# Kernel tuning notes

Hardware: AMD Instinct MI355X
Metric: run time of the kernel (lower is better)

## Reference

```python
import jax, jax.numpy as jnp
import numpy as np

EMBED = 256
HEADS = 8
LEVELS = 3
POINTS = 4
MLP = 4
SS = np.array([[100, 100], [50, 50], [25, 25]], np.int32)  # (H, W) per level


def setup_inputs() -> dict:
    key = jax.random.key(0)
    ks = jax.random.split(key, 12)
    B, Q = 2, 128 * 128
    NV = int((SS[:, 0] * SS[:, 1]).sum())
    C = EMBED
    F = C * MLP
    s = 0.02

    def w(k, shape):
        return jax.random.normal(k, shape, jnp.float32) * s

    return dict(
        query=jax.random.normal(ks[0], (B, Q, C), jnp.float32),
        value=jax.random.normal(ks[1], (B, NV, C), jnp.float32),
        query_pos=jax.random.normal(ks[2], (B, Q, C), jnp.float32),
        ref_pts=jax.random.uniform(ks[3], (B, Q, 2), jnp.float32),
        spatial_shapes=SS,
        level_start_index=np.concatenate([[0], np.cumsum(SS[:, 0] * SS[:, 1])[:-1]]).astype(np.int32),
        ln1_g=jnp.ones(C), ln1_b=jnp.zeros(C),
        ln2_g=jnp.ones(C), ln2_b=jnp.zeros(C),
        W_value=w(ks[4], (C, C)), b_value=jnp.zeros(C),
        W_off=w(ks[5], (C, HEADS * LEVELS * POINTS * 2)), b_off=w(ks[6], (HEADS * LEVELS * POINTS * 2,)),
        W_attn=w(ks[7], (C, HEADS * LEVELS * POINTS)), b_attn=jnp.zeros(HEADS * LEVELS * POINTS),
        W_out=w(ks[8], (C, C)), b_out=jnp.zeros(C),
        W_ffn1=w(ks[9], (C, F)), b_ffn1=jnp.zeros(F),
        W_ffn2=w(ks[10], (F, C)), b_ffn2=jnp.zeros(C),
    )


def _layernorm(x, g, b, eps=1e-5):
    m = x.mean(-1, keepdims=True)
    v = ((x - m) ** 2).mean(-1, keepdims=True)
    return (x - m) * jax.lax.rsqrt(v + eps) * g + b


def _bilinear(v, loc, Hl, Wl):
    # v: [BH, Hl*Wl, d]; loc: [BH, Q, P, 2] normalized to [0,1].
    # grid_sample(align_corners=False, padding=zeros): pixel = loc*size - 0.5
    BH, Q, P, _ = loc.shape
    d = v.shape[-1]
    x = loc[..., 0] * Wl - 0.5
    y = loc[..., 1] * Hl - 0.5
    x0f = jnp.floor(x)
    y0f = jnp.floor(y)
    lx = x - x0f
    ly = y - y0f
    x0 = x0f.astype(jnp.int32)
    y0 = y0f.astype(jnp.int32)

    def gather(xi, yi):
        valid = ((xi >= 0) & (xi < Wl) & (yi >= 0) & (yi < Hl)).astype(v.dtype)
        idx = jnp.clip(yi, 0, Hl - 1) * Wl + jnp.clip(xi, 0, Wl - 1)
        g = jnp.take_along_axis(v, idx.reshape(BH, Q * P, 1), axis=1).reshape(BH, Q, P, d)
        return g * valid[..., None]

    w00 = (1 - lx) * (1 - ly)
    w01 = lx * (1 - ly)
    w10 = (1 - lx) * ly
    w11 = lx * ly
    return (gather(x0, y0) * w00[..., None] + gather(x0 + 1, y0) * w01[..., None]
            + gather(x0, y0 + 1) * w10[..., None] + gather(x0 + 1, y0 + 1) * w11[..., None])


def _forward(query, value, query_pos, ref_pts, spatial_shapes,
             ln1_g, ln1_b, ln2_g, ln2_b,
             W_value, b_value, W_off, b_off, W_attn, b_attn, W_out, b_out,
             W_ffn1, b_ffn1, W_ffn2, b_ffn2):
    B, Q, C = query.shape
    Hh, L, P = HEADS, LEVELS, POINTS
    d = C // Hh
    ss = np.asarray(spatial_shapes)
    starts = np.concatenate([[0], np.cumsum(ss[:, 0] * ss[:, 1])])

    # pre-norm + positional embedding (MSDeformAttn adds query_pos)
    qn = _layernorm(query, ln1_g, ln1_b)
    q = qn + query_pos

    # value projection, split heads
    v = (value @ W_value + b_value).reshape(B, -1, Hh, d)

    off = (q @ W_off + b_off).reshape(B, Q, Hh, L, P, 2)
    aw = jax.nn.softmax((q @ W_attn + b_attn).reshape(B, Q, Hh, L * P), axis=-1)
    aw = aw.reshape(B, Q, Hh, L, P)

    # offset normalizer is (W, H) per level
    normalizer = jnp.asarray(ss[:, ::-1].copy(), jnp.float32)
    # bev_value path: ref_pts broadcast over levels
    loc = ref_pts[:, :, None, None, None, :] + off / normalizer[None, None, None, :, None, :]

    out = jnp.zeros((B * Hh, Q, d), query.dtype)
    for l in range(L):
        Hl, Wl = int(ss[l, 0]), int(ss[l, 1])
        v_l = v[:, starts[l]:starts[l + 1]].transpose(0, 2, 1, 3).reshape(B * Hh, Hl * Wl, d)
        loc_l = loc[:, :, :, l].transpose(0, 2, 1, 3, 4).reshape(B * Hh, Q, P, 2)
        sampled = _bilinear(v_l, loc_l, Hl, Wl)  # [BH, Q, P, d]
        w_l = aw[:, :, :, l].transpose(0, 2, 1, 3).reshape(B * Hh, Q, P)
        out = out + (sampled * w_l[..., None]).sum(2)

    out = out.reshape(B, Hh, Q, d).transpose(0, 2, 1, 3).reshape(B, Q, C)
    x = query + (out @ W_out + b_out)

    h = _layernorm(x, ln2_g, ln2_b)
    x = x + (jax.nn.gelu(h @ W_ffn1 + b_ffn1, approximate=False) @ W_ffn2 + b_ffn2)
    return x


def reference(query, value, query_pos, ref_pts, spatial_shapes, level_start_index,
              ln1_g, ln1_b, ln2_g, ln2_b,
              W_value, b_value, W_off, b_off, W_attn, b_attn, W_out, b_out,
              W_ffn1, b_ffn1, W_ffn2, b_ffn2):
    return _forward(query, value, query_pos, ref_pts, spatial_shapes,
                    ln1_g, ln1_b, ln2_g, ln2_b,
                    W_value, b_value, W_off, b_off, W_attn, b_attn, W_out, b_out,
                    W_ffn1, b_ffn1, W_ffn2, b_ffn2)
```

## Files before the change

### kernel.cpp

```cpp
#include <hip/hip_runtime.h>
#include <hip/hip_bf16.h>

#define BQ      2
#define QLEN    16384
#define CDIM    256
#define HEADS   8
#define LEV     3
#define PTS     4
#define DHEAD   32
#define NVTOT   13125
#define FDIM    1024
#define NTOK    (BQ*QLEN)
#define MROWS_V (BQ*NVTOT)
#define NPROJ   288

typedef __attribute__((ext_vector_type(8))) short short8;
typedef __attribute__((ext_vector_type(4))) float floatx4;
typedef unsigned long long u64;

typedef const __attribute__((address_space(1))) unsigned int gu32;
typedef __attribute__((address_space(3))) unsigned int lu32;

__device__ __forceinline__ int imin(int a, int b){ return a<b?a:b; }
__device__ __forceinline__ int imax(int a, int b){ return a>b?a:b; }

__device__ __forceinline__ float bf2f(unsigned short u){ return __uint_as_float((unsigned)u << 16); }
__device__ __forceinline__ unsigned short f2bf(float f)
{
    __hip_bfloat16 h = __float2bfloat16(f);
    return *(unsigned short*)&h;
}
__device__ __forceinline__ u64 pack4(float4 v)
{
    return (u64)f2bf(v.x) | ((u64)f2bf(v.y) << 16)
         | ((u64)f2bf(v.z) << 32) | ((u64)f2bf(v.w) << 48);
}
__device__ __forceinline__ float4 unpack4(u64 c)
{
    float4 v;
    v.x = bf2f((unsigned short)(c));
    v.y = bf2f((unsigned short)(c >> 16));
    v.z = bf2f((unsigned short)(c >> 32));
    v.w = bf2f((unsigned short)(c >> 48));
    return v;
}

__device__ __forceinline__ float gelu_f(float x)
{
    float u2 = x * x;
    float a  = x * fmaf(0.0713548163f, u2, 1.5957691216f);
    float e  = __expf(a);
    float r  = __builtin_amdgcn_rcpf(e + 1.0f);
    return fmaf(-x, r, x);
}

__device__ __forceinline__ void ln_core(float4 v, const float* __restrict__ pos, int tok,
                                        const float* __restrict__ g, const float* __restrict__ b,
                                        int lane, __hip_bfloat16* __restrict__ out)
{
    float s = v.x + v.y + v.z + v.w;
    #pragma unroll
    for (int o = 32; o > 0; o >>= 1) s += __shfl_down(s, o);
    s = __shfl(s, 0);
    float mean = s * (1.0f / 256.0f);
    float4 c; c.x = v.x - mean; c.y = v.y - mean; c.z = v.z - mean; c.w = v.w - mean;
    float q2 = c.x*c.x + c.y*c.y + c.z*c.z + c.w*c.w;
    #pragma unroll
    for (int o = 32; o > 0; o >>= 1) q2 += __shfl_down(q2, o);
    q2 = __shfl(q2, 0);
    float rstd = rsqrtf(q2 * (1.0f / 256.0f) + 1e-5f);
    float4 gg = ((const float4*)g)[lane];
    float4 bb = ((const float4*)b)[lane];
    float4 o4;
    o4.x = c.x * rstd * gg.x + bb.x;
    o4.y = c.y * rstd * gg.y + bb.y;
    o4.z = c.z * rstd * gg.z + bb.z;
    o4.w = c.w * rstd * gg.w + bb.w;
    if (pos) {
        float4 p = ((const float4*)(pos + (size_t)tok * CDIM))[lane];
        o4.x += p.x; o4.y += p.y; o4.z += p.z; o4.w += p.w;
    }
    *(u64*)(out + (size_t)tok * CDIM + lane * 4) = pack4(o4);
}

#define WT_BLOCKS  2946
#define CVT_BLOCKS 6563
#define LN_BLOCKS  8192

__global__ __launch_bounds__(256)
void prep_k(const float* __restrict__ Wv,  const float* __restrict__ Woff,
            const float* __restrict__ Wat, const float* __restrict__ Wout,
            const float* __restrict__ W1,  const float* __restrict__ W2,
            const float* __restrict__ boff, const float* __restrict__ bat,
            const float* __restrict__ value, const float* __restrict__ query,
            const float* __restrict__ qpos,  const float* __restrict__ ln1g,
            const float* __restrict__ ln1b,
            __hip_bfloat16* __restrict__ o_v,  __hip_bfloat16* __restrict__ o_c,
            __hip_bfloat16* __restrict__ o_out,
            __hip_bfloat16* __restrict__ o_1,  __hip_bfloat16* __restrict__ o_2,
            float* __restrict__ o_bc,
            __hip_bfloat16* __restrict__ vbf,  __hip_bfloat16* __restrict__ qbf)
{
    int bx = blockIdx.x;
    if (bx < WT_BLOCKS) {
        int gid = bx * 256 + threadIdx.x;
        if (gid < 65536) {
            int idx = gid, n = idx >> 8, k = idx & 255;
            o_v[idx] = __float2bfloat16(Wv[(size_t)k * 256 + n]);
        } else if (gid < 163840) {
            int idx = gid - 65536, n = idx >> 8, k = idx & 255;
            float v = 0.0f;
            if (n < 192)       v = Woff[(size_t)k * 192 + n];
            else if (n < 288)  v = Wat[(size_t)k * 96 + (n - 192)];
            o_c[idx] = __float2bfloat16(v);
        } else if (gid < 229376) {
            int idx = gid - 163840, n = idx >> 8, k = idx & 255;
            o_out[idx] = __float2bfloat16(Wout[(size_t)k * 256 + n]);
        } else if (gid < 491520) {
            int idx = gid - 229376, n = idx >> 8, k = idx & 255;
            o_1[idx] = __float2bfloat16(W1[(size_t)k * 1024 + n]);
        } else if (gid < 753664) {
            int idx = gid - 491520, n = idx >> 10, k = idx & 1023;
            o_2[idx] = __float2bfloat16(W2[(size_t)k * 256 + n]);
        } else if (gid < 753952) {
            int idx = gid - 753664;
            o_bc[idx] = (idx < 192) ? boff[idx] : bat[idx - 192];
        }
    } else if (bx < WT_BLOCKS + CVT_BLOCKS) {
        int i = (bx - WT_BLOCKS) * 256 + threadIdx.x;
        if (i < MROWS_V * CDIM / 4) {
            float4 v = ((const float4*)value)[i];
            *(u64*)(vbf + (size_t)i * 4) = pack4(v);
        }
    } else {
        int tok  = (bx - WT_BLOCKS - CVT_BLOCKS) * 4 + (threadIdx.x >> 6);
        int lane = threadIdx.x & 63;
        float4 v = ((const float4*)(query + (size_t)tok * CDIM))[lane];
        ln_core(v, qpos, tok, ln1g, ln1b, lane, qbf);
    }
}

__global__ __launch_bounds__(256)
void ln2_k(const __hip_bfloat16* __restrict__ x, const float* __restrict__ g,
           const float* __restrict__ b, __hip_bfloat16* __restrict__ out)
{
    int tok  = blockIdx.x * 4 + (threadIdx.x >> 6);
    int lane = threadIdx.x & 63;
    float4 v = unpack4(((const u64*)(x + (size_t)tok * CDIM))[lane]);
    ln_core(v, nullptr, tok, g, b, lane, out);
}

enum { EP_PLAIN_BF16 = 0, EP_GELU_BF16 = 1, EP_RES_F2BF = 2, EP_RES_BF2F = 3 };

__global__ __launch_bounds__(256)
void mm_k(const __hip_bfloat16* __restrict__ A, const __hip_bfloat16* __restrict__ Bt,
          const float* __restrict__ bias, const void* __restrict__ res,
          void* __restrict__ Cout, int M, int N, int K, int mode)
{
    __shared__ float4 smem4[2048];
    __hip_bfloat16* Ws = (__hip_bfloat16*)smem4;
    __hip_bfloat16* Ts = (__hip_bfloat16*)smem4 + 128*64;
    u64* st = (u64*)smem4;
    int t = threadIdx.x;
    int lane = t & 63;
    int wave = t >> 6;
    int wm = wave >> 1, wn = wave & 1;
    int lm = lane & 15, lk = lane >> 4;
    int m0 = blockIdx.x * 128;
    int n0 = blockIdx.y * 128;

    floatx4 acc[4][4];
    #pragma unroll
    for (int i = 0; i < 4; i++)
        #pragma unroll
        for (int j = 0; j < 4; j++) acc[i][j] = (floatx4)0.0f;

    for (int kt = 0; kt < K; kt += 64) {
        #pragma unroll
        for (int i = 0; i < 4; i++) {
            int cc  = i * 256 + t;
            int row = cc >> 3;
            int c   = cc & 7;
            int kc  = c ^ (row & 7);
            int ra  = m0 + row; if (ra >= M) ra = M - 1;
            const __hip_bfloat16* gw = Bt + (size_t)(n0 + row) * K + kt + kc * 8;
            const __hip_bfloat16* gt = A  + (size_t)ra * K + kt + kc * 8;
            __builtin_amdgcn_global_load_lds((gu32*)gw, (lu32*)(Ws + cc * 8), 16, 0, 0);
            __builtin_amdgcn_global_load_lds((gu32*)gt, (lu32*)(Ts + cc * 8), 16, 0, 0);
        }
        __syncthreads();
        #pragma unroll
        for (int ks = 0; ks < 2; ks++) {
            short8 wf[4], tf[4];
            #pragma unroll
            for (int i = 0; i < 4; i++) {
                int rw = wn * 64 + i * 16 + lm;
                int cw = (ks * 4 + lk) ^ (rw & 7);
                wf[i] = *(const short8*)(Ws + (rw * 8 + cw) * 8);
                int rt = wm * 64 + i * 16 + lm;
                int ct = (ks * 4 + lk) ^ (rt & 7);
                tf[i] = *(const short8*)(Ts + (rt * 8 + ct) * 8);
            }
            #pragma unroll
            for (int i = 0; i < 4; i++)
                #pragma unroll
                for (int j = 0; j < 4; j++)
                    acc[i][j] = __builtin_amdgcn_mfma_f32_16x16x32_bf16(wf[i], tf[j], acc[i][j], 0, 0, 0);
        }
        __syncthreads();
    }

    #pragma unroll
    for (int i = 0; i < 4; i++) {
        int chan = n0 + wn * 64 + i * 16 + lk * 4;
        float4 b4 = make_float4(0.f, 0.f, 0.f, 0.f);
        if (chan < N) b4 = *(const float4*)(bias + chan);
        int c4 = wn * 16 + i * 4 + lk;
        #pragma unroll
        for (int j = 0; j < 4; j++) {
            int tl = wm * 64 + j * 16 + lm;
            float4 v;
            v.x = acc[i][j][0] + b4.x;
            v.y = acc[i][j][1] + b4.y;
            v.z = acc[i][j][2] + b4.z;
            v.w = acc[i][j][3] + b4.w;
            st[tl * 32 + (c4 ^ (tl & 31))] = pack4(v);
        }
    }
    __syncthreads();

    int rel = (t & 31) * 4;
    int c4r = t & 31;
    #pragma unroll
    for (int it = 0; it < 16; it++) {
        int tl   = it * 8 + (t >> 5);
        int tok  = m0 + tl;
        int chan = n0 + rel;
        if (tok >= M || chan >= N) continue;
        u64 chunk = st[tl * 32 + (c4r ^ (tl & 31))];
        if (mode == EP_PLAIN_BF16) {
            *(u64*)((__hip_bfloat16*)Cout + (size_t)tok * N + chan) = chunk;
        } else if (mode == EP_GELU_BF16) {
            float4 v = unpack4(chunk);
            v.x = gelu_f(v.x); v.y = gelu_f(v.y); v.z = gelu_f(v.z); v.w = gelu_f(v.w);
            *(u64*)((__hip_bfloat16*)Cout + (size_t)tok * N + chan) = pack4(v);
        } else if (mode == EP_RES_F2BF) {
            float4 v = unpack4(chunk);
            float4 rr = *(const float4*)((const float*)res + (size_t)tok * N + chan);
            v.x += rr.x; v.y += rr.y; v.z += rr.z; v.w += rr.w;
            *(u64*)((__hip_bfloat16*)Cout + (size_t)tok * N + chan) = pack4(v);
        } else {
            float4 v = unpack4(chunk);
            float4 rr = unpack4(*(const u64*)((const __hip_bfloat16*)res + (size_t)tok * N + chan));
            v.x += rr.x; v.y += rr.y; v.z += rr.z; v.w += rr.w;
            *(float4*)((float*)Cout + (size_t)tok * N + chan) = v;
        }
    }
}

__global__ __launch_bounds__(256)
void sample_k(const __hip_bfloat16* __restrict__ v, const __hip_bfloat16* __restrict__ cbuf,
              const float* __restrict__ ref, __hip_bfloat16* __restrict__ out)
{
    __shared__ int4   metaIdx[4 * 104];
    __shared__ float4 metaW[4 * 104];

    int wid  = threadIdx.x >> 6;
    int lane = threadIdx.x & 63;
    int t    = blockIdx.x * 4 + wid;
    int b    = t >> 14;
    float rx = ref[(size_t)t * 2 + 0];
    float ry = ref[(size_t)t * 2 + 1];
    const __hip_bfloat16* crow = cbuf + (size_t)t * NPROJ;

    #pragma unroll
    for (int rnd = 0; rnd < 2; rnd++) {
        int slot = rnd * 64 + lane;
        int h = slot >> 4, p = slot & 15;
        int pc = imin(p, 11);
        unsigned upk = *(const unsigned*)(crow + h * 24 + pc * 2);
        float ox = bf2f((unsigned short)upk);
        float oy = bf2f((unsigned short)(upk >> 16));
        float logit = bf2f(*(const unsigned short*)(crow + 192 + h * 12 + pc));
        float mx = logit;
        #pragma unroll
        for (int o = 8; o > 0; o >>= 1) mx = fmaxf(mx, __shfl_xor(mx, o, 16));
        float e = (p < 12) ? __expf(logit - mx) : 0.0f;
        float ssum = e;
        #pragma unroll
        for (int o = 8; o > 0; o >>= 1) ssum += __shfl_xor(ssum, o, 16);
        float aw = e * __builtin_amdgcn_rcpf(ssum);

        if (p < 12) {
            int l = p >> 2;
            float fS = (l == 0) ? 100.0f : ((l == 1) ? 50.0f : 25.0f);
            int   Wl = (l == 0) ? 100 : ((l == 1) ? 50 : 25);
            int   st = (l == 0) ? 0 : ((l == 1) ? 10000 : 12500);
            float x = fmaf(rx, fS, ox) - 0.5f;
            float y = fmaf(ry, fS, oy) - 0.5f;
            float x0f = floorf(x), y0f = floorf(y);
            float fx = x - x0f, fy = y - y0f;
            int x0 = (int)x0f, y0 = (int)y0f;
            int x1 = x0 + 1,  y1 = y0 + 1;
            int cx0 = imin(imax(x0, 0), Wl - 1), cx1 = imin(imax(x1, 0), Wl - 1);
            int cy0 = imin(imax(y0, 0), Wl - 1), cy1 = imin(imax(y1, 0), Wl - 1);
            float vx0 = (x0 >= 0 && x0 < Wl) ? 1.0f : 0.0f;
            float vx1 = (x1 >= 0 && x1 < Wl) ? 1.0f : 0.0f;
            float vy0 = (y0 >= 0 && y0 < Wl) ? 1.0f : 0.0f;
            float vy1 = (y1 >= 0 && y1 < Wl) ? 1.0f : 0.0f;
            int s = wid * 104 + h * 13 + p;
            metaIdx[s] = make_int4((st + cy0 * Wl + cx0) << 9, (st + cy0 * Wl + cx1) << 9,
                                   (st + cy1 * Wl + cx0) << 9, (st + cy1 * Wl + cx1) << 9);
            metaW[s] = make_float4((1.0f - fx) * (1.0f - fy) * aw * vx0 * vy0,
                                   fx * (1.0f - fy) * aw * vx1 * vy0,
                                   (1.0f - fx) * fy * aw * vx0 * vy1,
                                   fx * fy * aw * vx1 * vy1);
        }
    }
    __syncthreads();

    int h  = lane >> 3;
    int bs = __builtin_amdgcn_readfirstlane(b);
    const char* vb = (const char*)(v + (size_t)bs * NVTOT * CDIM);
    int hoff = lane * 8;
    float4 acc = {0.0f, 0.0f, 0.0f, 0.0f};
    #pragma unroll
    for (int p = 0; p < 12; p++) {
        int s = wid * 104 + h * 13 + p;
        int4   mi = metaIdx[s];
        float4 mw = metaW[s];
        u64 g0 = *(const u64*)(vb + (unsigned)(mi.x + hoff));
        u64 g1 = *(const u64*)(vb + (unsigned)(mi.y + hoff));
        u64 g2 = *(const u64*)(vb + (unsigned)(mi.z + hoff));
        u64 g3 = *(const u64*)(vb + (unsigned)(mi.w + hoff));
        {
            unsigned d0 = (unsigned)g0, d1 = (unsigned)(g0 >> 32);
            acc.x = fmaf(mw.x, __uint_as_float(d0 << 16), acc.x);
            acc.y = fmaf(mw.x, __uint_as_float(d0 & 0xffff0000u), acc.y);
            acc.z = fmaf(mw.x, __uint_as_float(d1 << 16), acc.z);
            acc.w = fmaf(mw.x, __uint_as_float(d1 & 0xffff0000u), acc.w);
        }
        {
            unsigned d0 = (unsigned)g1, d1 = (unsigned)(g1 >> 32);
            acc.x = fmaf(mw.y, __uint_as_float(d0 << 16), acc.x);
            acc.y = fmaf(mw.y, __uint_as_float(d0 & 0xffff0000u), acc.y);
            acc.z = fmaf(mw.y, __uint_as_float(d1 << 16), acc.z);
            acc.w = fmaf(mw.y, __uint_as_float(d1 & 0xffff0000u), acc.w);
        }
        {
            unsigned d0 = (unsigned)g2, d1 = (unsigned)(g2 >> 32);
            acc.x = fmaf(mw.z, __uint_as_float(d0 << 16), acc.x);
            acc.y = fmaf(mw.z, __uint_as_float(d0 & 0xffff0000u), acc.y);
            acc.z = fmaf(mw.z, __uint_as_float(d1 << 16), acc.z);
            acc.w = fmaf(mw.z, __uint_as_float(d1 & 0xffff0000u), acc.w);
        }
        {
            unsigned d0 = (unsigned)g3, d1 = (unsigned)(g3 >> 32);
            acc.x = fmaf(mw.w, __uint_as_float(d0 << 16), acc.x);
            acc.y = fmaf(mw.w, __uint_as_float(d0 & 0xffff0000u), acc.y);
            acc.z = fmaf(mw.w, __uint_as_float(d1 << 16), acc.z);
            acc.w = fmaf(mw.w, __uint_as_float(d1 & 0xffff0000u), acc.w);
        }
    }
    *(u64*)(out + (size_t)t * CDIM + lane * 4) = pack4(acc);
}

extern "C" void kernel_launch(void* const* d_in, const int* in_sizes, int n_in,
                              void* d_out, int out_size, void* d_ws, size_t ws_size,
                              hipStream_t stream)
{
    const float* query = (const float*)d_in[0];
    const float* value = (const float*)d_in[1];
    const float* qpos  = (const float*)d_in[2];
    const float* ref   = (const float*)d_in[3];
    const float* ln1g  = (const float*)d_in[6];
    const float* ln1b  = (const float*)d_in[7];
    const float* ln2g  = (const float*)d_in[8];
    const float* ln2b  = (const float*)d_in[9];
    const float* Wv    = (const float*)d_in[10];
    const float* bv    = (const float*)d_in[11];
    const float* Woff  = (const float*)d_in[12];
    const float* boff  = (const float*)d_in[13];
    const float* Wat   = (const float*)d_in[14];
    const float* bat   = (const float*)d_in[15];
    const float* Wout  = (const float*)d_in[16];
    const float* bout  = (const float*)d_in[17];
    const float* W1    = (const float*)d_in[18];
    const float* b1    = (const float*)d_in[19];
    const float* W2    = (const float*)d_in[20];
    const float* b2    = (const float*)d_in[21];
    float* out = (float*)d_out;
    char*  ws  = (char*)d_ws;

    const size_t MB = 1024 * 1024;
    __hip_bfloat16* Wvt   = (__hip_bfloat16*)(ws + 0);
    __hip_bfloat16* Wct   = (__hip_bfloat16*)(ws + 131072);
    __hip_bfloat16* Woutt = (__hip_bfloat16*)(ws + 327680);
    __hip_bfloat16* W1t   = (__hip_bfloat16*)(ws + 458752);
    __hip_bfloat16* W2t   = (__hip_bfloat16*)(ws + 983040);
    float*          bcomb = (float*)(ws + 1507328);
    __hip_bfloat16* qbf   = (__hip_bfloat16*)(ws + 2  * MB);
    __hip_bfloat16* aoutb = (__hip_bfloat16*)(ws + 19 * MB);
    __hip_bfloat16* vbf   = (__hip_bfloat16*)(ws + 36 * MB);
    __hip_bfloat16* vbuf  = (__hip_bfloat16*)(ws + 50 * MB);
    __hip_bfloat16* xbf   = (__hip_bfloat16*)(ws + 64 * MB);
    __hip_bfloat16* cbuf  = (__hip_bfloat16*)(ws + 81 * MB);
    __hip_bfloat16* gbf   = (__hip_bfloat16*)(ws + 100 * MB);
    __hip_bfloat16* hbf   = qbf;

    prep_k<<<WT_BLOCKS + CVT_BLOCKS + LN_BLOCKS, 256, 0, stream>>>(
        Wv, Woff, Wat, Wout, W1, W2, boff, bat, value, query, qpos, ln1g, ln1b,
        Wvt, Wct, Woutt, W1t, W2t, bcomb, vbf, qbf);
    mm_k<<<dim3((MROWS_V + 127) / 128, 2), 256, 0, stream>>>(
        vbf, Wvt, bv, nullptr, vbuf, MROWS_V, 256, 256, EP_PLAIN_BF16);
    mm_k<<<dim3(NTOK / 128, 3), 256, 0, stream>>>(
        qbf, Wct, bcomb, nullptr, cbuf, NTOK, NPROJ, 256, EP_PLAIN_BF16);
    sample_k<<<NTOK / 4, 256, 0, stream>>>(vbuf, cbuf, ref, aoutb);
    mm_k<<<dim3(NTOK / 128, 2), 256, 0, stream>>>(
        aoutb, Woutt, bout, query, xbf, NTOK, 256, 256, EP_RES_F2BF);
    ln2_k<<<NTOK / 4, 256, 0, stream>>>(xbf, ln2g, ln2b, hbf);
    mm_k<<<dim3(NTOK / 128, 8), 256, 0, stream>>>(
        hbf, W1t, b1, nullptr, gbf, NTOK, FDIM, 256, EP_GELU_BF16);
    mm_k<<<dim3(NTOK / 128, 2), 256, 0, stream>>>(
        gbf, W2t, b2, xbf, out, NTOK, 256, 1024, EP_RES_BF2F);
}
```

Before: 347.8 us.

## Fuse output projection with residual and LayerNorm2; software-pipeline sampler gathers

Replaces the output-projection GEMM plus the separate LN2 kernel with one 512-thread kernel that computes a full 256-wide row tile, adds the fp32 residual and applies LayerNorm in-block. It writes both the bf16 residual stream and the normalized activations. This removes one launch and a round trip of the bf16 x buffer through memory. The sampler's bilinear gathers are also triple-buffered, prefetching three points ahead to hide gather latency, and it gets a minimum-occupancy launch bound. The costs are more registers and higher LDS use per block in the fused kernel, and LN2 now reads the fp32 sum before rounding.

```diff
diff --git a/kernel.cpp b/kernel.cpp
--- a/kernel.cpp
+++ b/kernel.cpp
@@ -140,17 +140,7 @@
     }
 }
 
-__global__ __launch_bounds__(256)
-void ln2_k(const __hip_bfloat16* __restrict__ x, const float* __restrict__ g,
-           const float* __restrict__ b, __hip_bfloat16* __restrict__ out)
-{
-    int tok  = blockIdx.x * 4 + (threadIdx.x >> 6);
-    int lane = threadIdx.x & 63;
-    float4 v = unpack4(((const u64*)(x + (size_t)tok * CDIM))[lane]);
-    ln_core(v, nullptr, tok, g, b, lane, out);
-}
-
-enum { EP_PLAIN_BF16 = 0, EP_GELU_BF16 = 1, EP_RES_F2BF = 2, EP_RES_BF2F = 3 };
+enum { EP_PLAIN_BF16 = 0, EP_GELU_BF16 = 1, EP_RES_BF2F = 3 };
 
 __global__ __launch_bounds__(256)
 void mm_k(const __hip_bfloat16* __restrict__ A, const __hip_bfloat16* __restrict__ Bt,
@@ -244,11 +234,6 @@
             float4 v = unpack4(chunk);
             v.x = gelu_f(v.x); v.y = gelu_f(v.y); v.z = gelu_f(v.z); v.w = gelu_f(v.w);
             *(u64*)((__hip_bfloat16*)Cout + (size_t)tok * N + chan) = pack4(v);
-        } else if (mode == EP_RES_F2BF) {
-            float4 v = unpack4(chunk);
-            float4 rr = *(const float4*)((const float*)res + (size_t)tok * N + chan);
-            v.x += rr.x; v.y += rr.y; v.z += rr.z; v.w += rr.w;
-            *(u64*)((__hip_bfloat16*)Cout + (size_t)tok * N + chan) = pack4(v);
         } else {
             float4 v = unpack4(chunk);
             float4 rr = unpack4(*(const u64*)((const __hip_bfloat16*)res + (size_t)tok * N + chan));
@@ -258,7 +243,125 @@
     }
 }
 
-__global__ __launch_bounds__(256)
+__global__ __launch_bounds__(512)
+void mmln_k(const __hip_bfloat16* __restrict__ A, const __hip_bfloat16* __restrict__ Bt,
+            const float* __restrict__ bias, const float* __restrict__ res,
+            const float* __restrict__ g2, const float* __restrict__ b2,
+            __hip_bfloat16* __restrict__ xout, __hip_bfloat16* __restrict__ hout)
+{
+    __shared__ char smemraw[65536];
+    __hip_bfloat16* Ws = (__hip_bfloat16*)smemraw;
+    __hip_bfloat16* Ts = (__hip_bfloat16*)smemraw + 256 * 64;
+    u64* st = (u64*)smemraw;
+    int t = threadIdx.x;
+    int lane = t & 63;
+    int wave = t >> 6;
+    int wm = wave >> 2;
+    int wn = wave & 3;
+    int lm = lane & 15, lk = lane >> 4;
+    int m0 = blockIdx.x * 128;
+
+    floatx4 acc[4][4];
+    #pragma unroll
+    for (int i = 0; i < 4; i++)
+        #pragma unroll
+        for (int j = 0; j < 4; j++) acc[i][j] = (floatx4)0.0f;
+
+    for (int kt = 0; kt < 256; kt += 64) {
+        #pragma unroll
+        for (int i = 0; i < 6; i++) {
+            int cc = i * 512 + t;
+            if (cc < 2048) {
+                int row = cc >> 3, c = cc & 7;
+                int kc = c ^ (row & 7);
+                const __hip_bfloat16* gw = Bt + (size_t)row * 256 + kt + kc * 8;
+                __builtin_amdgcn_global_load_lds((gu32*)gw, (lu32*)(Ws + cc * 8), 16, 0, 0);
+            } else {
+                int cc2 = cc - 2048;
+                int row = cc2 >> 3, c = cc2 & 7;
+                int kc = c ^ (row & 7);
+                const __hip_bfloat16* gt = A + (size_t)(m0 + row) * 256 + kt + kc * 8;
+                __builtin_amdgcn_global_load_lds((gu32*)gt, (lu32*)(Ts + cc2 * 8), 16, 0, 0);
+            }
+        }
+        __syncthreads();
+        #pragma unroll
+        for (int ks = 0; ks < 2; ks++) {
+            short8 wf[4], tf[4];
+            #pragma unroll
+            for (int i = 0; i < 4; i++) {
+                int rw = wn * 64 + i * 16 + lm;
+                int cw = (ks * 4 + lk) ^ (rw & 7);
+                wf[i] = *(const short8*)(Ws + (rw * 8 + cw) * 8);
+                int rt = wm * 64 + i * 16 + lm;
+                int ct = (ks * 4 + lk) ^ (rt & 7);
+                tf[i] = *(const short8*)(Ts + (rt * 8 + ct) * 8);
+            }
+            #pragma unroll
+            for (int i = 0; i < 4; i++)
+                #pragma unroll
+                for (int j = 0; j < 4; j++)
+                    acc[i][j] = __builtin_amdgcn_mfma_f32_16x16x32_bf16(wf[i], tf[j], acc[i][j], 0, 0, 0);
+        }
+        __syncthreads();
+    }
+
+    #pragma unroll
+    for (int i = 0; i < 4; i++) {
+        int chan = wn * 64 + i * 16 + lk * 4;
+        float4 b4 = *(const float4*)(bias + chan);
+        int c4 = chan >> 2;
+        #pragma unroll
+        for (int j = 0; j < 4; j++) {
+            int tl = wm * 64 + j * 16 + lm;
+            float4 v;
+            v.x = acc[i][j][0] + b4.x;
+            v.y = acc[i][j][1] + b4.y;
+            v.z = acc[i][j][2] + b4.z;
+            v.w = acc[i][j][3] + b4.w;
+            st[tl * 64 + (c4 ^ (tl & 63))] = pack4(v);
+        }
+    }
+    __syncthreads();
+
+    int tl = t >> 2;
+    int qq = t & 3;
+    int tok = m0 + tl;
+    const float4* rq = (const float4*)(res + (size_t)tok * 256 + qq * 64);
+    float4 x[16];
+    float s1 = 0.0f, s2 = 0.0f;
+    #pragma unroll
+    for (int u = 0; u < 16; u++) {
+        float4 v = unpack4(st[tl * 64 + ((qq * 16 + u) ^ (tl & 63))]);
+        float4 rr = rq[u];
+        v.x += rr.x; v.y += rr.y; v.z += rr.z; v.w += rr.w;
+        x[u] = v;
+        s1 += v.x + v.y + v.z + v.w;
+        s2 += v.x * v.x + v.y * v.y + v.z * v.z + v.w * v.w;
+    }
+    s1 += __shfl_xor(s1, 1); s1 += __shfl_xor(s1, 2);
+    s2 += __shfl_xor(s2, 1); s2 += __shfl_xor(s2, 2);
+    float mean = s1 * (1.0f / 256.0f);
+    float var  = s2 * (1.0f / 256.0f) - mean * mean;
+    float rstd = rsqrtf(var + 1e-5f);
+    __hip_bfloat16* xp = xout + (size_t)tok * 256 + qq * 64;
+    __hip_bfloat16* hp = hout + (size_t)tok * 256 + qq * 64;
+    const float4* g4 = (const float4*)(g2 + qq * 64);
+    const float4* b4p = (const float4*)(b2 + qq * 64);
+    #pragma unroll
+    for (int u = 0; u < 16; u++) {
+        *(u64*)(xp + u * 4) = pack4(x[u]);
+        float4 gg = g4[u], bb = b4p[u];
+        float4 h;
+        h.x = (x[u].x - mean) * rstd * gg.x + bb.x;
+        h.y = (x[u].y - mean) * rstd * gg.y + bb.y;
+        h.z = (x[u].z - mean) * rstd * gg.z + bb.z;
+        h.w = (x[u].w - mean) * rstd * gg.w + bb.w;
+        *(u64*)(hp + u * 4) = pack4(h);
+    }
+}
+
+__global__ __launch_bounds__(256, 4)
 void sample_k(const __hip_bfloat16* __restrict__ v, const __hip_bfloat16* __restrict__ cbuf,
               const float* __restrict__ ref, __hip_bfloat16* __restrict__ out)
 {
@@ -323,39 +426,53 @@
     int bs = __builtin_amdgcn_readfirstlane(b);
     const char* vb = (const char*)(v + (size_t)bs * NVTOT * CDIM);
     int hoff = lane * 8;
+    int sbase = wid * 104 + h * 13;
     float4 acc = {0.0f, 0.0f, 0.0f, 0.0f};
+
+    u64 gg[3][4];
+    #pragma unroll
+    for (int pp = 0; pp < 3; pp++) {
+        int4 mi = metaIdx[sbase + pp];
+        gg[pp][0] = *(const u64*)(vb + (unsigned)(mi.x + hoff));
+        gg[pp][1] = *(const u64*)(vb + (unsigned)(mi.y + hoff));
+        gg[pp][2] = *(const u64*)(vb + (unsigned)(mi.z + hoff));
+        gg[pp][3] = *(const u64*)(vb + (unsigned)(mi.w + hoff));
+    }
     #pragma unroll
     for (int p = 0; p < 12; p++) {
-        int s = wid * 104 + h * 13 + p;
-        int4   mi = metaIdx[s];
-        float4 mw = metaW[s];
-        u64 g0 = *(const u64*)(vb + (unsigned)(mi.x + hoff));
-        u64 g1 = *(const u64*)(vb + (unsigned)(mi.y + hoff));
-        u64 g2 = *(const u64*)(vb + (unsigned)(mi.z + hoff));
-        u64 g3 = *(const u64*)(vb + (unsigned)(mi.w + hoff));
+        int buf = p % 3;
+        float4 mw = metaW[sbase + p];
+        u64 c0 = gg[buf][0], c1 = gg[buf][1], c2 = gg[buf][2], c3 = gg[buf][3];
+        if (p + 3 < 12) {
+            int4 mi = metaIdx[sbase + p + 3];
+            gg[buf][0] = *(const u64*)(vb + (unsigned)(mi.x + hoff));
+            gg[buf][1] = *(const u64*)(vb + (unsigned)(mi.y + hoff));
+            gg[buf][2] = *(const u64*)(vb + (unsigned)(mi.z + hoff));
+            gg[buf][3] = *(const u64*)(vb + (unsigned)(mi.w + hoff));
+        }
         {
-            unsigned d0 = (unsigned)g0, d1 = (unsigned)(g0 >> 32);
+            unsigned d0 = (unsigned)c0, d1 = (unsigned)(c0 >> 32);
             acc.x = fmaf(mw.x, __uint_as_float(d0 << 16), acc.x);
             acc.y = fmaf(mw.x, __uint_as_float(d0 & 0xffff0000u), acc.y);
             acc.z = fmaf(mw.x, __uint_as_float(d1 << 16), acc.z);
             acc.w = fmaf(mw.x, __uint_as_float(d1 & 0xffff0000u), acc.w);
         }
         {
-            unsigned d0 = (unsigned)g1, d1 = (unsigned)(g1 >> 32);
+            unsigned d0 = (unsigned)c1, d1 = (unsigned)(c1 >> 32);
             acc.x = fmaf(mw.y, __uint_as_float(d0 << 16), acc.x);
             acc.y = fmaf(mw.y, __uint_as_float(d0 & 0xffff0000u), acc.y);
             acc.z = fmaf(mw.y, __uint_as_float(d1 << 16), acc.z);
             acc.w = fmaf(mw.y, __uint_as_float(d1 & 0xffff0000u), acc.w);
         }
         {
-            unsigned d0 = (unsigned)g2, d1 = (unsigned)(g2 >> 32);
+            unsigned d0 = (unsigned)c2, d1 = (unsigned)(c2 >> 32);
             acc.x = fmaf(mw.z, __uint_as_float(d0 << 16), acc.x);
             acc.y = fmaf(mw.z, __uint_as_float(d0 & 0xffff0000u), acc.y);
             acc.z = fmaf(mw.z, __uint_as_float(d1 << 16), acc.z);
             acc.w = fmaf(mw.z, __uint_as_float(d1 & 0xffff0000u), acc.w);
         }
         {
-            unsigned d0 = (unsigned)g3, d1 = (unsigned)(g3 >> 32);
+            unsigned d0 = (unsigned)c3, d1 = (unsigned)(c3 >> 32);
             acc.x = fmaf(mw.w, __uint_as_float(d0 << 16), acc.x);
             acc.y = fmaf(mw.w, __uint_as_float(d0 & 0xffff0000u), acc.y);
             acc.z = fmaf(mw.w, __uint_as_float(d1 << 16), acc.z);
@@ -416,9 +533,8 @@
     mm_k<<<dim3(NTOK / 128, 3), 256, 0, stream>>>(
         qbf, Wct, bcomb, nullptr, cbuf, NTOK, NPROJ, 256, EP_PLAIN_BF16);
     sample_k<<<NTOK / 4, 256, 0, stream>>>(vbuf, cbuf, ref, aoutb);
-    mm_k<<<dim3(NTOK / 128, 2), 256, 0, stream>>>(
-        aoutb, Woutt, bout, query, xbf, NTOK, 256, 256, EP_RES_F2BF);
-    ln2_k<<<NTOK / 4, 256, 0, stream>>>(xbf, ln2g, ln2b, hbf);
+    mmln_k<<<NTOK / 128, 512, 0, stream>>>(
+        aoutb, Woutt, bout, query, ln2g, ln2b, xbf, hbf);
     mm_k<<<dim3(NTOK / 128, 8), 256, 0, stream>>>(
         hbf, W1t, b1, nullptr, gbf, NTOK, FDIM, 256, EP_GELU_BF16);
     mm_k<<<dim3(NTOK / 128, 2), 256, 0, stream>>>(
```

After: 374.4 us. 7.7% more time.
